# Kernel tuning notes

Measured on AMD Instinct MI355X. Metric: run time of the kernel, lower is better.

Reference implementation:

```python
import jax, jax.numpy as jnp
import numpy as np

T, D, H, HD = 4096, 1536, 12, 128  # tokens, hidden, heads, head_dim
NEG = -1e9


def rotate_half(x):
    x1, x2 = jnp.split(x, 2, axis=-1)
    return jnp.concatenate((-x2, x1), axis=-1)


def setup_inputs() -> dict:
    key = jax.random.key(0)
    k1, k2, k3, k4 = jax.random.split(key, 4)
    hidden_states = jax.random.normal(k1, (T, D), dtype=jnp.float32)
    cu_seqlens = (jnp.arange(5, dtype=jnp.int32) * (T // 4))  # [0,1024,2048,3072,4096]
    # rotary angles: positions within each segment times inverse frequencies
    pos = jnp.arange(T, dtype=jnp.float32) % (T // 4)
    inv_freq = 1.0 / (10000.0 ** (jnp.arange(0, HD // 2, dtype=jnp.float32) / (HD // 2)))
    rotary_pos_emb = pos[:, None] * inv_freq[None, :]  # (T, HD//2)
    w_qkv = jax.random.normal(k2, (3 * D, D), dtype=jnp.float32) * (D ** -0.5)
    w_proj = jax.random.normal(k3, (D, D), dtype=jnp.float32) * (D ** -0.5)
    return {"hidden_states": hidden_states, "cu_seqlens": cu_seqlens,
            "rotary_pos_emb": rotary_pos_emb, "w_qkv": w_qkv, "w_proj": w_proj}


def reference(hidden_states, cu_seqlens, rotary_pos_emb, w_qkv, w_proj):
    seq_len = hidden_states.shape[0]
    scaling = HD ** -0.5
    # fused QKV projection: (T, 3D) -> (3, T, H, HD)
    qkv = (hidden_states @ w_qkv.T).reshape(seq_len, 3, H, HD).transpose(1, 0, 2, 3)
    q, k, v = qkv[0], qkv[1], qkv[2]
    # RoPE (vision style): emb = cat(rpe, rpe) along last dim
    emb = jnp.concatenate((rotary_pos_emb, rotary_pos_emb), axis=-1)  # (T, HD)
    cos = jnp.cos(emb)[:, None, :]  # (T, 1, HD) broadcast over heads
    sin = jnp.sin(emb)[:, None, :]
    q = q * cos + rotate_half(q) * sin
    k = k * cos + rotate_half(k) * sin
    # block-diagonal mask from cu_seqlens (varlen packing)
    seg_id = jnp.searchsorted(cu_seqlens[1:], jnp.arange(seq_len), side="right")
    block_mask = seg_id[:, None] == seg_id[None, :]  # (T, T) bool
    # attention per head: (H, T, HD)
    qh = q.transpose(1, 0, 2)
    kh = k.transpose(1, 0, 2)
    vh = v.transpose(1, 0, 2)
    scores = jnp.einsum("htd,hsd->hts", qh, kh) * scaling
    scores = jnp.where(block_mask[None, :, :], scores, NEG)
    attn = jax.nn.softmax(scores, axis=-1)
    out = jnp.einsum("hts,hsd->htd", attn, vh)  # (H, T, HD)
    out = out.transpose(1, 0, 2).reshape(seq_len, D)
    return out @ w_proj.T


if __name__ == "__main__":
    o = reference(**setup_inputs())
    print(o.shape, o.dtype)
```

## Files before the change

### kernel.cpp

```cpp
#include <hip/hip_runtime.h>
#include <stdint.h>

#define TT 4096
#define DD 1536
#define NH 12
#define HD_ 128

typedef __bf16 bf16x8 __attribute__((ext_vector_type(8)));
typedef float  f32x4  __attribute__((ext_vector_type(4)));
typedef float  f32x16 __attribute__((ext_vector_type(16)));

__device__ __forceinline__ unsigned short f2b(float f) {
  union { float f; uint32_t u; } x; x.f = f;
  uint32_t r = x.u + 0x7fffu + ((x.u >> 16) & 1u);
  return (unsigned short)(r >> 16);
}
__device__ __forceinline__ float b2f(unsigned short b) {
  union { uint32_t u; float f; } x; x.u = ((uint32_t)b) << 16;
  return x.f;
}

__device__ __forceinline__ f32x16 mfma32(bf16x8 a, bf16x8 b, f32x16 c) {
  return __builtin_amdgcn_mfma_f32_32x32x16_bf16(a, b, c, 0, 0, 0);
}

__device__ __forceinline__ void async16(const void* g, void* l) {
  __builtin_amdgcn_global_load_lds((const __attribute__((address_space(1))) uint32_t*)g,
                                   (__attribute__((address_space(3))) uint32_t*)l,
                                   16, 0, 0);
}

__global__ void cast_bf16_kernel(const float* __restrict__ in,
                                 unsigned short* __restrict__ out, int n) {
  int i = (blockIdx.x * blockDim.x + threadIdx.x) * 4;
  if (i + 3 < n) {
    float4 v = *reinterpret_cast<const float4*>(in + i);
    ushort4 o;
    o.x = f2b(v.x); o.y = f2b(v.y); o.z = f2b(v.z); o.w = f2b(v.w);
    *reinterpret_cast<ushort4*>(out + i) = o;
  }
}

__global__ void trig_table_kernel(const float* __restrict__ rpe,
                                  float* __restrict__ cs, float* __restrict__ sn) {
  int i = blockIdx.x * blockDim.x + threadIdx.x;
  float e = rpe[i];
  float s, c;
  sincosf(e, &s, &c);
  cs[i] = c;
  sn[i] = s;
}

__global__ __launch_bounds__(256, 4) void gemm_qkv_kernel(
    const unsigned short* __restrict__ A, const unsigned short* __restrict__ B,
    unsigned short* __restrict__ Qp, unsigned short* __restrict__ Kp,
    unsigned short* __restrict__ Vt, const float* __restrict__ csT,
    const float* __restrict__ snT) {
  __shared__ char smem[16384];
  unsigned short* lA = (unsigned short*)smem;
  unsigned short* lB = (unsigned short*)(smem + 8192);
  float* Lf = (float*)smem;

  const int tid = threadIdx.x;
  const int lane = tid & 63;
  const int wave = tid >> 6;
  const int wm = wave >> 1, wn = wave & 1;
  const int lr = lane & 15, lh = lane >> 4;

  const int m0 = blockIdx.x * 128;
  const int n0 = blockIdx.y * 128;

  const unsigned short* Ag = A + (size_t)(m0 + (tid >> 2)) * DD + (tid & 3) * 8;
  const unsigned short* Bg = B + (size_t)(n0 + (tid >> 2)) * DD + (tid & 3) * 8;
  f32x4 acc[4][4] = {};
  for (int k0 = 0; k0 < DD; k0 += 32) {
    async16(Ag + k0, &lA[tid * 8]);
    async16(Ag + k0 + (size_t)64 * DD, &lA[2048 + tid * 8]);
    async16(Bg + k0, &lB[tid * 8]);
    async16(Bg + k0 + (size_t)64 * DD, &lB[2048 + tid * 8]);
    __syncthreads();
    bf16x8 af[4], bfr[4];
#pragma unroll
    for (int i = 0; i < 4; i++) {
      af[i]  = *reinterpret_cast<const bf16x8*>(&lA[(wm * 64 + i * 16 + lr) * 32 + lh * 8]);
      bfr[i] = *reinterpret_cast<const bf16x8*>(&lB[(wn * 64 + i * 16 + lr) * 32 + lh * 8]);
    }
#pragma unroll
    for (int i = 0; i < 4; i++)
#pragma unroll
      for (int j = 0; j < 4; j++)
        acc[i][j] = __builtin_amdgcn_mfma_f32_16x16x32_bf16(af[i], bfr[j], acc[i][j], 0, 0, 0);
    __syncthreads();
  }

  const int s  = n0 / DD;
  const int hh = (n0 - s * DD) >> 7;

  if (s == 2) {
#pragma unroll
    for (int i = 0; i < 4; i++)
#pragma unroll
      for (int j = 0; j < 4; j++) {
        const int dd = wn * 64 + j * 16 + lr;
        const int t0 = m0 + wm * 64 + i * 16 + lh * 4;
        ushort4 st;
        st.x = f2b(acc[i][j][0]); st.y = f2b(acc[i][j][1]);
        st.z = f2b(acc[i][j][2]); st.w = f2b(acc[i][j][3]);
        *reinterpret_cast<ushort4*>(&Vt[((size_t)(hh * HD_ + dd)) * TT + t0]) = st;
      }
  } else {
    unsigned short* dst = (s == 0) ? Qp : Kp;
    const float scale =
        (s == 0) ? (0.08838834764831845f * 1.4426950408889634f) : 1.0f;
#pragma unroll
    for (int i = 0; i < 4; i++) {
      __syncthreads();
#pragma unroll
      for (int j = 0; j < 4; j++)
#pragma unroll
        for (int r = 0; r < 4; r++)
          Lf[(wm * 16 + lh * 4 + r) * 128 + wn * 64 + j * 16 + lr] = acc[i][j][r];
      __syncthreads();
#pragma unroll
      for (int j = 0; j < 4; j++) {
        const int dd = wn * 64 + j * 16 + lr;
        const int d2 = dd & 63;
        const float sgn = (dd < 64) ? -1.f : 1.f;
#pragma unroll
        for (int r = 0; r < 4; r++) {
          const int lrow = wm * 16 + lh * 4 + r;
          const int t = m0 + wm * 64 + i * 16 + lh * 4 + r;
          const float own = acc[i][j][r];
          const float par = Lf[lrow * 128 + (dd ^ 64)];
          const float c = csT[t * 64 + d2];
          const float sn_ = snT[t * 64 + d2];
          dst[((size_t)hh * TT + t) * HD_ + dd] =
              f2b((own * c + sgn * par * sn_) * scale);
        }
        __builtin_amdgcn_sched_barrier(0);
      }
    }
  }
}

__global__ __launch_bounds__(512) void attn_kernel(
    const unsigned short* __restrict__ Qp, const unsigned short* __restrict__ Kp,
    const unsigned short* __restrict__ Vt, const int* __restrict__ cu,
    unsigned short* __restrict__ AO) {
  __shared__ unsigned short lds[32768];
  const int bid = blockIdx.x;
  const int tid = threadIdx.x;
  const int wave = tid >> 6;
  const int lane = tid & 63;
  const int lq = lane & 31;
  const int hi = lane >> 5;
  const int swz = lq & 7;

  const int xcd  = bid & 7;
  const int idx  = bid >> 3;
  const int pair = xcd * 6 + (idx >> 2);
  const int qblk = idx & 3;
  const int h    = pair >> 2;
  const int seg  = pair & 3;
  const int kstart = cu[seg], kend = cu[seg + 1];
  const int q0 = kstart + (qblk * 8 + wave) * 32;

  const unsigned short* Kh = Kp + (size_t)h * TT * HD_;
  const unsigned short* Vh = Vt + (size_t)h * HD_ * TT;

  const int krow0 = tid >> 4, kc0 = tid & 15;
  const int vrow0 = tid >> 3, vc0 = tid & 7;

#define STAGE_TILE(BUF, KT)                                                    \
  {                                                                            \
    unsigned short* Lk = &lds[(BUF) * 16384];                                  \
    unsigned short* Lv = Lk + 8192;                                            \
    _Pragma("unroll")                                                          \
    for (int r = 0; r < 2; r++) {                                              \
      int row = krow0 + r * 32;                                                \
      int c = kc0 ^ (row & 7);                                                 \
      async16(Kh + (size_t)((KT) + row) * HD_ + c * 8, Lk + tid * 8 + r * 4096); \
    }                                                                          \
    _Pragma("unroll")                                                          \
    for (int r = 0; r < 2; r++) {                                              \
      int row = vrow0 + r * 64;                                                \
      int c = vc0 ^ (row & 7);                                                 \
      async16(Vh + (size_t)row * TT + (KT) + c * 8, Lv + tid * 8 + r * 4096);  \
    }                                                                          \
  }

  const unsigned short* Qg = Qp + ((size_t)h * TT + q0 + lq) * HD_ + hi * 8;
  bf16x8 qf[8];
#pragma unroll
  for (int s = 0; s < 8; s++)
    qf[s] = *reinterpret_cast<const bf16x8*>(Qg + s * 16);

  STAGE_TILE(0, kstart);
  __syncthreads();

  f32x16 o0 = {}, o1 = {}, o2 = {}, o3 = {};
  float lsum = 0.f;
  int cur = 0;

  for (int kt = kstart; kt < kend; kt += 64) {
    const int ktn = (kt + 64 < kend) ? (kt + 64) : kt;
    STAGE_TILE(cur ^ 1, ktn);

    const unsigned short* Kl = &lds[cur * 16384];
    const unsigned short* Vl = Kl + 8192;

    f32x16 sA = {}, sB = {};
#pragma unroll
    for (int s = 0; s < 8; s++) {
      bf16x8 kf = *reinterpret_cast<const bf16x8*>(
          Kl + lq * 128 + (((s << 1) | hi) ^ swz) * 8);
      sA = mfma32(kf, qf[s], sA);
    }
#pragma unroll
    for (int s = 0; s < 8; s++) {
      bf16x8 kf = *reinterpret_cast<const bf16x8*>(
          Kl + 4096 + lq * 128 + (((s << 1) | hi) ^ swz) * 8);
      sB = mfma32(kf, qf[s], sB);
    }

    bf16x8 pfrag[4];
    float acc0 = 0.f, acc1 = 0.f;
#pragma unroll
    for (int g = 0; g < 4; g++) {
      const f32x16 S = (g & 2) ? sB : sA;
      const int b = (g & 1) * 8;
      float e0 = __builtin_amdgcn_exp2f(S[b + 0]);
      float e1 = __builtin_amdgcn_exp2f(S[b + 1]);
      float e2 = __builtin_amdgcn_exp2f(S[b + 2]);
      float e3 = __builtin_amdgcn_exp2f(S[b + 3]);
      float e4 = __builtin_amdgcn_exp2f(S[b + 4]);
      float e5 = __builtin_amdgcn_exp2f(S[b + 5]);
      float e6 = __builtin_amdgcn_exp2f(S[b + 6]);
      float e7 = __builtin_amdgcn_exp2f(S[b + 7]);
      acc0 += (e0 + e1) + (e2 + e3);
      acc1 += (e4 + e5) + (e6 + e7);
      union PW { uint32_t u; __bf16 e[2]; } p0, p1, p2, p3;
      p0.e[0] = (__bf16)e0; p0.e[1] = (__bf16)e1;
      p1.e[0] = (__bf16)e2; p1.e[1] = (__bf16)e3;
      p2.e[0] = (__bf16)e4; p2.e[1] = (__bf16)e5;
      p3.e[0] = (__bf16)e6; p3.e[1] = (__bf16)e7;
      uint32_t W2 = (uint32_t)__shfl_xor((int)(hi ? p0.u : p2.u), 32);
      uint32_t W3 = (uint32_t)__shfl_xor((int)(hi ? p1.u : p3.u), 32);
      union F { uint32_t w[4]; bf16x8 v; } f;
      f.w[0] = hi ? W2 : p0.u;
      f.w[1] = hi ? W3 : p1.u;
      f.w[2] = hi ? p2.u : W2;
      f.w[3] = hi ? p3.u : W3;
      pfrag[g] = f.v;
    }
    float tsum = acc0 + acc1;
    lsum += tsum + __shfl_xor(tsum, 32);

#pragma unroll
    for (int g = 0; g < 4; g++) {
      const int co = (((g << 1) | hi) ^ swz) * 8;
      bf16x8 v0 = *reinterpret_cast<const bf16x8*>(Vl + (lq)       * 64 + co);
      bf16x8 v1 = *reinterpret_cast<const bf16x8*>(Vl + (32 + lq)  * 64 + co);
      bf16x8 v2 = *reinterpret_cast<const bf16x8*>(Vl + (64 + lq)  * 64 + co);
      bf16x8 v3 = *reinterpret_cast<const bf16x8*>(Vl + (96 + lq)  * 64 + co);
      o0 = mfma32(v0, pfrag[g], o0);
      o1 = mfma32(v1, pfrag[g], o1);
      o2 = mfma32(v2, pfrag[g], o2);
      o3 = mfma32(v3, pfrag[g], o3);
    }

    __syncthreads();
    cur ^= 1;
  }
#undef STAGE_TILE

  const float inv = 1.0f / lsum;
  unsigned short* Ab = AO + (size_t)(q0 + lq) * DD + h * HD_ + 4 * hi;
#pragma unroll
  for (int dblk = 0; dblk < 4; dblk++) {
    f32x16 o = (dblk == 0) ? o0 : (dblk == 1) ? o1 : (dblk == 2) ? o2 : o3;
#pragma unroll
    for (int rq = 0; rq < 4; rq++) {
      ushort4 st;
      st.x = f2b(o[rq * 4 + 0] * inv);
      st.y = f2b(o[rq * 4 + 1] * inv);
      st.z = f2b(o[rq * 4 + 2] * inv);
      st.w = f2b(o[rq * 4 + 3] * inv);
      *reinterpret_cast<ushort4*>(Ab + dblk * 32 + rq * 8) = st;
    }
  }
}

__global__ __launch_bounds__(256) void gemm_out_kernel(
    const unsigned short* __restrict__ A, const unsigned short* __restrict__ B,
    float* __restrict__ C) {
  __shared__ unsigned short lA[128 * 32];
  __shared__ unsigned short lB[128 * 32];
  const int tid = threadIdx.x;
  const int lane = tid & 63;
  const int wave = tid >> 6;
  const int wm = wave >> 1, wn = wave & 1;
  const int lr = lane & 15, lh = lane >> 4;
  const int m0 = blockIdx.x * 128, n0 = blockIdx.y * 128;
  const unsigned short* Ag = A + (size_t)(m0 + (tid >> 2)) * DD + (tid & 3) * 8;
  const unsigned short* Bg = B + (size_t)(n0 + (tid >> 2)) * DD + (tid & 3) * 8;
  f32x4 acc[4][4] = {};
  for (int k0 = 0; k0 < DD; k0 += 32) {
    async16(Ag + k0, &lA[tid * 8]);
    async16(Ag + k0 + (size_t)64 * DD, &lA[2048 + tid * 8]);
    async16(Bg + k0, &lB[tid * 8]);
    async16(Bg + k0 + (size_t)64 * DD, &lB[2048 + tid * 8]);
    __syncthreads();
    bf16x8 af[4], bfr[4];
#pragma unroll
    for (int i = 0; i < 4; i++) {
      af[i]  = *reinterpret_cast<const bf16x8*>(&lA[(wm * 64 + i * 16 + lr) * 32 + lh * 8]);
      bfr[i] = *reinterpret_cast<const bf16x8*>(&lB[(wn * 64 + i * 16 + lr) * 32 + lh * 8]);
    }
#pragma unroll
    for (int i = 0; i < 4; i++)
#pragma unroll
      for (int j = 0; j < 4; j++)
        acc[i][j] = __builtin_amdgcn_mfma_f32_16x16x32_bf16(af[i], bfr[j], acc[i][j], 0, 0, 0);
    __syncthreads();
  }
#pragma unroll
  for (int i = 0; i < 4; i++)
#pragma unroll
    for (int j = 0; j < 4; j++) {
      int cn = n0 + wn * 64 + j * 16 + lr;
#pragma unroll
      for (int r = 0; r < 4; r++) {
        int t = m0 + wm * 64 + i * 16 + lh * 4 + r;
        C[(size_t)t * DD + cn] = acc[i][j][r];
      }
    }
}

extern "C" void kernel_launch(void* const* d_in, const int* in_sizes, int n_in,
                              void* d_out, int out_size, void* d_ws, size_t ws_size,
                              hipStream_t stream) {
  const float* hs    = (const float*)d_in[0];
  const int*   cu    = (const int*)d_in[1];
  const float* rpe   = (const float*)d_in[2];
  const float* wqkv  = (const float*)d_in[3];
  const float* wproj = (const float*)d_in[4];
  float* out = (float*)d_out;
  char* ws = (char*)d_ws;

  unsigned short* hb = (unsigned short*)(ws + 0);
  unsigned short* wq = (unsigned short*)(ws + 12582912);
  unsigned short* wp = (unsigned short*)(ws + 26738688);
  unsigned short* Qp = (unsigned short*)(ws + 31457280);
  unsigned short* Kp = (unsigned short*)(ws + 44040192);
  unsigned short* Vt = (unsigned short*)(ws + 56623104);

  float* csT = (float*)wp;
  float* snT = csT + TT * 64;

  trig_table_kernel<<<1024, 256, 0, stream>>>(rpe, csT, snT);
  cast_bf16_kernel<<<6144, 256, 0, stream>>>(hs, hb, TT * DD);
  cast_bf16_kernel<<<6912, 256, 0, stream>>>(wqkv, wq, 3 * DD * DD);

  gemm_qkv_kernel<<<dim3(32, 36), 256, 0, stream>>>(hb, wq, Qp, Kp, Vt, csT, snT);

  cast_bf16_kernel<<<2304, 256, 0, stream>>>(wproj, wp, DD * DD);

  attn_kernel<<<192, 512, 0, stream>>>(Qp, Kp, Vt, cu, hb );

  gemm_out_kernel<<<dim3(32, 12), 256, 0, stream>>>(hb , wp, out);
}
```

Baseline: 190.4 us.

## Double-buffer LDS in both GEMMs and keep RoPE partner in registers

Both the QKV and output projection GEMMs now use two LDS buffers, issuing the async global-to-LDS loads for the next K tile before computing the current one. This removes one barrier per iteration and lets copies overlap the MFMAs. The QKV kernel also remaps its B-tile columns so each wave holds both halves of the rotary pair in registers, which removes the LDS round trip and its extra barriers in the RoPE epilogue. The output GEMM gains a minimum-occupancy launch bound. Doubling LDS to 32KB per block may lower occupancy, and the last iteration issues a redundant reload.

```diff
diff --git a/kernel.cpp b/kernel.cpp
--- a/kernel.cpp
+++ b/kernel.cpp
@@ -56,11 +56,7 @@
     unsigned short* __restrict__ Qp, unsigned short* __restrict__ Kp,
     unsigned short* __restrict__ Vt, const float* __restrict__ csT,
     const float* __restrict__ snT) {
-  __shared__ char smem[16384];
-  unsigned short* lA = (unsigned short*)smem;
-  unsigned short* lB = (unsigned short*)(smem + 8192);
-  float* Lf = (float*)smem;
-
+  __shared__ char smem[32768];
   const int tid = threadIdx.x;
   const int lane = tid & 63;
   const int wave = tid >> 6;
@@ -72,18 +68,31 @@
 
   const unsigned short* Ag = A + (size_t)(m0 + (tid >> 2)) * DD + (tid & 3) * 8;
   const unsigned short* Bg = B + (size_t)(n0 + (tid >> 2)) * DD + (tid & 3) * 8;
+
+#define STAGE_G(BUF, K0)                                            \
+  {                                                                 \
+    unsigned short* la = (unsigned short*)(smem + (BUF) * 16384);   \
+    unsigned short* lb = la + 4096;                                 \
+    async16(Ag + (K0), &la[tid * 8]);                               \
+    async16(Ag + (K0) + (size_t)64 * DD, &la[2048 + tid * 8]);      \
+    async16(Bg + (K0), &lb[tid * 8]);                               \
+    async16(Bg + (K0) + (size_t)64 * DD, &lb[2048 + tid * 8]);      \
+  }
+
   f32x4 acc[4][4] = {};
+  STAGE_G(0, 0);
+  __syncthreads();
+  int cur = 0;
   for (int k0 = 0; k0 < DD; k0 += 32) {
-    async16(Ag + k0, &lA[tid * 8]);
-    async16(Ag + k0 + (size_t)64 * DD, &lA[2048 + tid * 8]);
-    async16(Bg + k0, &lB[tid * 8]);
-    async16(Bg + k0 + (size_t)64 * DD, &lB[2048 + tid * 8]);
-    __syncthreads();
+    const int kn = (k0 + 32 < DD) ? (k0 + 32) : k0;
+    STAGE_G(cur ^ 1, kn);
+    const unsigned short* la = (const unsigned short*)(smem + cur * 16384);
+    const unsigned short* lb = la + 4096;
     bf16x8 af[4], bfr[4];
 #pragma unroll
     for (int i = 0; i < 4; i++) {
-      af[i]  = *reinterpret_cast<const bf16x8*>(&lA[(wm * 64 + i * 16 + lr) * 32 + lh * 8]);
-      bfr[i] = *reinterpret_cast<const bf16x8*>(&lB[(wn * 64 + i * 16 + lr) * 32 + lh * 8]);
+      af[i]  = *reinterpret_cast<const bf16x8*>(&la[(wm * 64 + i * 16 + lr) * 32 + lh * 8]);
+      bfr[i] = *reinterpret_cast<const bf16x8*>(&lb[(i * 32 + wn * 16 + lr) * 32 + lh * 8]);
     }
 #pragma unroll
     for (int i = 0; i < 4; i++)
@@ -91,7 +100,9 @@
       for (int j = 0; j < 4; j++)
         acc[i][j] = __builtin_amdgcn_mfma_f32_16x16x32_bf16(af[i], bfr[j], acc[i][j], 0, 0, 0);
     __syncthreads();
-  }
+    cur ^= 1;
+  }
+#undef STAGE_G
 
   const int s  = n0 / DD;
   const int hh = (n0 - s * DD) >> 7;
@@ -101,7 +112,7 @@
     for (int i = 0; i < 4; i++)
 #pragma unroll
       for (int j = 0; j < 4; j++) {
-        const int dd = wn * 64 + j * 16 + lr;
+        const int dd = j * 32 + wn * 16 + lr;
         const int t0 = m0 + wm * 64 + i * 16 + lh * 4;
         ushort4 st;
         st.x = f2b(acc[i][j][0]); st.y = f2b(acc[i][j][1]);
@@ -114,25 +125,17 @@
         (s == 0) ? (0.08838834764831845f * 1.4426950408889634f) : 1.0f;
 #pragma unroll
     for (int i = 0; i < 4; i++) {
-      __syncthreads();
-#pragma unroll
-      for (int j = 0; j < 4; j++)
-#pragma unroll
-        for (int r = 0; r < 4; r++)
-          Lf[(wm * 16 + lh * 4 + r) * 128 + wn * 64 + j * 16 + lr] = acc[i][j][r];
-      __syncthreads();
 #pragma unroll
       for (int j = 0; j < 4; j++) {
-        const int dd = wn * 64 + j * 16 + lr;
+        const int dd = j * 32 + wn * 16 + lr;
         const int d2 = dd & 63;
         const float sgn = (dd < 64) ? -1.f : 1.f;
 #pragma unroll
         for (int r = 0; r < 4; r++) {
-          const int lrow = wm * 16 + lh * 4 + r;
           const int t = m0 + wm * 64 + i * 16 + lh * 4 + r;
           const float own = acc[i][j][r];
-          const float par = Lf[lrow * 128 + (dd ^ 64)];
-          const float c = csT[t * 64 + d2];
+          const float par = acc[i][j ^ 2][r];
+          const float c   = csT[t * 64 + d2];
           const float sn_ = snT[t * 64 + d2];
           dst[((size_t)hh * TT + t) * HD_ + dd] =
               f2b((own * c + sgn * par * sn_) * scale);
@@ -291,11 +294,10 @@
   }
 }
 
-__global__ __launch_bounds__(256) void gemm_out_kernel(
+__global__ __launch_bounds__(256, 4) void gemm_out_kernel(
     const unsigned short* __restrict__ A, const unsigned short* __restrict__ B,
     float* __restrict__ C) {
-  __shared__ unsigned short lA[128 * 32];
-  __shared__ unsigned short lB[128 * 32];
+  __shared__ char smem[32768];
   const int tid = threadIdx.x;
   const int lane = tid & 63;
   const int wave = tid >> 6;
@@ -304,18 +306,31 @@
   const int m0 = blockIdx.x * 128, n0 = blockIdx.y * 128;
   const unsigned short* Ag = A + (size_t)(m0 + (tid >> 2)) * DD + (tid & 3) * 8;
   const unsigned short* Bg = B + (size_t)(n0 + (tid >> 2)) * DD + (tid & 3) * 8;
+
+#define STAGE_G(BUF, K0)                                            \
+  {                                                                 \
+    unsigned short* la = (unsigned short*)(smem + (BUF) * 16384);   \
+    unsigned short* lb = la + 4096;                                 \
+    async16(Ag + (K0), &la[tid * 8]);                               \
+    async16(Ag + (K0) + (size_t)64 * DD, &la[2048 + tid * 8]);      \
+    async16(Bg + (K0), &lb[tid * 8]);                               \
+    async16(Bg + (K0) + (size_t)64 * DD, &lb[2048 + tid * 8]);      \
+  }
+
   f32x4 acc[4][4] = {};
+  STAGE_G(0, 0);
+  __syncthreads();
+  int cur = 0;
   for (int k0 = 0; k0 < DD; k0 += 32) {
-    async16(Ag + k0, &lA[tid * 8]);
-    async16(Ag + k0 + (size_t)64 * DD, &lA[2048 + tid * 8]);
-    async16(Bg + k0, &lB[tid * 8]);
-    async16(Bg + k0 + (size_t)64 * DD, &lB[2048 + tid * 8]);
-    __syncthreads();
+    const int kn = (k0 + 32 < DD) ? (k0 + 32) : k0;
+    STAGE_G(cur ^ 1, kn);
+    const unsigned short* la = (const unsigned short*)(smem + cur * 16384);
+    const unsigned short* lb = la + 4096;
     bf16x8 af[4], bfr[4];
 #pragma unroll
     for (int i = 0; i < 4; i++) {
-      af[i]  = *reinterpret_cast<const bf16x8*>(&lA[(wm * 64 + i * 16 + lr) * 32 + lh * 8]);
-      bfr[i] = *reinterpret_cast<const bf16x8*>(&lB[(wn * 64 + i * 16 + lr) * 32 + lh * 8]);
+      af[i]  = *reinterpret_cast<const bf16x8*>(&la[(wm * 64 + i * 16 + lr) * 32 + lh * 8]);
+      bfr[i] = *reinterpret_cast<const bf16x8*>(&lb[(wn * 64 + i * 16 + lr) * 32 + lh * 8]);
     }
 #pragma unroll
     for (int i = 0; i < 4; i++)
@@ -323,7 +338,10 @@
       for (int j = 0; j < 4; j++)
         acc[i][j] = __builtin_amdgcn_mfma_f32_16x16x32_bf16(af[i], bfr[j], acc[i][j], 0, 0, 0);
     __syncthreads();
-  }
+    cur ^= 1;
+  }
+#undef STAGE_G
+
 #pragma unroll
   for (int i = 0; i < 4; i++)
 #pragma unroll
```

Result: faster. 174.5 us (-8.4%).
